# Kernel optimization log

Measured on AMD Instinct MI355X. Metric: run time of the kernel, lower is better.

## Reference

```python
import jax, jax.numpy as jnp
import numpy as np

HEATMAP_SIZE = 64

def _gauss5():
    n = np.array([[1, 4, 7, 4, 1],
                  [4, 16, 26, 16, 4],
                  [7, 26, 41, 26, 7],
                  [4, 16, 26, 16, 4],
                  [1, 4, 7, 4, 1]], dtype=np.float32) / 41.0
    return n

def setup_inputs() -> dict:
    key = jax.random.key(0)
    k1, k2, k3 = jax.random.split(key, 3)
    B, K = 1024, 24
    # coords in [-1.2, 1.2] so a few land out of the heatmap and exercise the masking path
    x = jax.random.uniform(k1, (B, K, 2), jnp.float32, -1.2, 1.2)
    # every (out,in) filter slice is the same 5x5 binomial gaussian (as in weights_init)
    weight = jnp.asarray(np.broadcast_to(_gauss5(), (K, K, 5, 5)).copy())
    vis_batch = jax.random.randint(k2, (256,), 0, B, jnp.int32)
    vis_kps = jax.random.randint(k3, (256,), 0, K, jnp.int32)
    return {"x": x, "weight": weight, "vis_batch": vis_batch, "vis_kps": vis_kps}

def _forward(x, weight, vis_batch, vis_kps):
    B, K, _ = x.shape
    H = HEATMAP_SIZE
    # j2d_resized = round((j2d + 1) / 2 * (H - 1)).long()
    coords = jnp.round((x + 1.0) * 0.5 * (H - 1)).astype(jnp.int32)  # [B,K,2] = (x,y)
    # rows with any out-of-range coord get both coords set to 0
    invalid = jnp.any((coords >= H) | (coords < 0), axis=-1)  # [B,K]
    coords = jnp.where(invalid[..., None], 0, coords)
    # torch quirk: only places a 1 where the x-coordinate is nonzero
    place = (coords[..., 0] != 0).astype(weight.dtype)  # [B,K]
    ohx = jax.nn.one_hot(coords[..., 0], H, dtype=weight.dtype)  # [B,K,H]
    ohy = jax.nn.one_hot(coords[..., 1], H, dtype=weight.dtype)  # [B,K,H]
    # sparse heatmap: 1 at (y, x)
    heat = place[..., None, None] * ohy[..., :, None] * ohx[..., None, :]  # [B,K,H,H]
    # heatmap[vis_batch, vis_kps, :, :] = 0
    kill = jnp.zeros((B, K), weight.dtype).at[vis_batch, vis_kps].set(1.0)
    heat = heat * (1.0 - kill)[..., None, None]
    # full 24->24 channel-mixing 5x5 conv, padding=2, no bias
    out = jax.lax.conv_general_dilated(
        heat, weight, window_strides=(1, 1), padding=((2, 2), (2, 2)),
        dimension_numbers=("NCHW", "OIHW", "NCHW"))
    return out

def reference(x, weight, vis_batch, vis_kps):
    return _forward(x, weight, vis_batch, vis_kps)
```

## Files before the change

### kernel.cpp

```cpp
#include <hip/hip_runtime.h>
#include <math.h>

#define B_SZ 1024
#define K_SZ 24
#define H_SZ 64
#define NVIS 256


__global__ __launch_bounds__(256) void gs_prep(
    const float2* __restrict__ x,
    const int*    __restrict__ vis_b,
    const int*    __restrict__ vis_k,
    int*          __restrict__ spike_tab)
{
    const int bk = blockIdx.x * 256 + threadIdx.x;
    const int b  = bk / K_SZ;
    const int k  = bk - b * K_SZ;
    const float2 c = x[bk];
    const int cx = (int)rintf((c.x + 1.0f) * 0.5f * 63.0f);
    const int cy = (int)rintf((c.y + 1.0f) * 0.5f * 63.0f);
    const bool ok = (cx >= 1) & (cx < H_SZ) & (cy >= 0) & (cy < H_SZ);
    int s = ok ? (cy * H_SZ + cx) : -1;
    for (int i = 0; i < NVIS; ++i) {
        if ((vis_b[i] == b) & (vis_k[i] == k)) s = -1;
    }
    spike_tab[bk] = s;
}

__global__ __launch_bounds__(256) void gs_main(
    const int*   __restrict__ spike_tab,
    const float* __restrict__ w,
    float*       __restrict__ out)
{
    __shared__ float tile[H_SZ * H_SZ];
    const int bid = blockIdx.x;
    const int b   = bid / K_SZ;
    const int o   = bid - b * K_SZ;
    const int tid = threadIdx.x;

    const int*   sp = spike_tab + b * K_SZ;
    const float* wo = w + o * (K_SZ * 25);
    int   sv[3]; float wv[3]; int pp[3];
    #pragma unroll
    for (int it = 0; it < 3; ++it) {
        const int t = tid + it * 256;
        if (t < K_SZ * 25) {
            const int c = t / 25;
            pp[it] = t - c * 25;
            sv[it] = sp[c];
            wv[it] = wo[t];
        } else {
            sv[it] = -1;
        }
    }

    float4* t4 = (float4*)tile;
    const float4 z = make_float4(0.f, 0.f, 0.f, 0.f);
    #pragma unroll
    for (int r = 0; r < 4; ++r) t4[r * 256 + tid] = z;
    __syncthreads();

    #pragma unroll
    for (int it = 0; it < 3; ++it) {
        const int s = sv[it];
        if (s >= 0) {
            const int y  = s >> 6;
            const int xx = s & 63;
            const int di = pp[it] / 5;
            const int dj = pp[it] - di * 5;
            const int i  = y + 2 - di;
            const int j  = xx + 2 - dj;
            if (((unsigned)i < H_SZ) & ((unsigned)j < H_SZ))
                atomicAdd(&tile[i * H_SZ + j], wv[it]);
        }
    }
    __syncthreads();

    float4* o4 = (float4*)(out + (size_t)bid * (H_SZ * H_SZ));
    #pragma unroll
    for (int r = 0; r < 4; ++r) o4[r * 256 + tid] = t4[r * 256 + tid];
}

extern "C" void kernel_launch(void* const* d_in, const int* in_sizes, int n_in,
                              void* d_out, int out_size, void* d_ws, size_t ws_size,
                              hipStream_t stream) {
    const float2* x     = (const float2*)d_in[0];
    const float*  w     = (const float*)d_in[1];
    const int*    vis_b = (const int*)d_in[2];
    const int*    vis_k = (const int*)d_in[3];
    float*        out   = (float*)d_out;
    int*          spike_tab = (int*)d_ws;

    gs_prep<<<(B_SZ * K_SZ) / 256, 256, 0, stream>>>(x, vis_b, vis_k, spike_tab);
    gs_main<<<B_SZ * K_SZ, 256, 0, stream>>>(spike_tab, w, out);
}
```

Measured before the change: 401.4 us.

## Process four output planes per block and stage kill list in shared memory

The main kernel now handles four output channels per block. It computes the spike scatter addresses once and reuses them across planes, zeroing and re-accumulating the shared tile for each plane. This cuts the block count by four and amortizes the address computation, but it adds extra barriers between planes. The prep kernel loads the kill list into shared memory as combined b*K+k indices, so each thread does one compare per entry instead of two global reads.

```diff
diff --git a/kernel.cpp b/kernel.cpp
--- a/kernel.cpp
+++ b/kernel.cpp
@@ -5,6 +5,7 @@
 #define K_SZ 24
 #define H_SZ 64
 #define NVIS 256
+#define PLANES 4
 
 
 __global__ __launch_bounds__(256) void gs_prep(
@@ -13,17 +14,19 @@
     const int*    __restrict__ vis_k,
     int*          __restrict__ spike_tab)
 {
-    const int bk = blockIdx.x * 256 + threadIdx.x;
-    const int b  = bk / K_SZ;
-    const int k  = bk - b * K_SZ;
+    __shared__ int kill[NVIS];
+    const int tid = threadIdx.x;
+    const int bk  = blockIdx.x * 256 + tid;
+    kill[tid] = vis_b[tid] * K_SZ + vis_k[tid];
     const float2 c = x[bk];
     const int cx = (int)rintf((c.x + 1.0f) * 0.5f * 63.0f);
     const int cy = (int)rintf((c.y + 1.0f) * 0.5f * 63.0f);
     const bool ok = (cx >= 1) & (cx < H_SZ) & (cy >= 0) & (cy < H_SZ);
     int s = ok ? (cy * H_SZ + cx) : -1;
-    for (int i = 0; i < NVIS; ++i) {
-        if ((vis_b[i] == b) & (vis_k[i] == k)) s = -1;
-    }
+    __syncthreads();
+#pragma unroll 16
+    for (int i = 0; i < NVIS; ++i)
+        if (kill[i] == bk) s = -1;
     spike_tab[bk] = s;
 }
 
@@ -34,51 +37,67 @@
 {
     __shared__ float tile[H_SZ * H_SZ];
     const int bid = blockIdx.x;
-    const int b   = bid / K_SZ;
-    const int o   = bid - b * K_SZ;
+    const int b   = bid / (K_SZ / PLANES);
+    const int o0  = (bid - b * (K_SZ / PLANES)) * PLANES;
     const int tid = threadIdx.x;
 
-    const int*   sp = spike_tab + b * K_SZ;
-    const float* wo = w + o * (K_SZ * 25);
-    int   sv[3]; float wv[3]; int pp[3];
-    #pragma unroll
+    const int* sp = spike_tab + b * K_SZ;
+    int addr[3];
+    int tt[3];
+#pragma unroll
     for (int it = 0; it < 3; ++it) {
         const int t = tid + it * 256;
+        addr[it] = -1;
+        tt[it]   = 0;
         if (t < K_SZ * 25) {
-            const int c = t / 25;
-            pp[it] = t - c * 25;
-            sv[it] = sp[c];
-            wv[it] = wo[t];
-        } else {
-            sv[it] = -1;
+            tt[it] = t;
+            const int c  = t / 25;
+            const int p  = t - c * 25;
+            const int s  = sp[c];
+            if (s >= 0) {
+                const int y  = s >> 6;
+                const int xx = s & 63;
+                const int di = p / 5;
+                const int dj = p - di * 5;
+                const int i  = y + 2 - di;
+                const int j  = xx + 2 - dj;
+                if (((unsigned)i < H_SZ) & ((unsigned)j < H_SZ))
+                    addr[it] = i * H_SZ + j;
+            }
         }
+    }
+
+    float wv[PLANES][3];
+#pragma unroll
+    for (int p = 0; p < PLANES; ++p) {
+        const float* wo = w + (o0 + p) * (K_SZ * 25);
+#pragma unroll
+        for (int it = 0; it < 3; ++it) wv[p][it] = wo[tt[it]];
     }
 
     float4* t4 = (float4*)tile;
     const float4 z = make_float4(0.f, 0.f, 0.f, 0.f);
-    #pragma unroll
+#pragma unroll
     for (int r = 0; r < 4; ++r) t4[r * 256 + tid] = z;
     __syncthreads();
 
-    #pragma unroll
-    for (int it = 0; it < 3; ++it) {
-        const int s = sv[it];
-        if (s >= 0) {
-            const int y  = s >> 6;
-            const int xx = s & 63;
-            const int di = pp[it] / 5;
-            const int dj = pp[it] - di * 5;
-            const int i  = y + 2 - di;
-            const int j  = xx + 2 - dj;
-            if (((unsigned)i < H_SZ) & ((unsigned)j < H_SZ))
-                atomicAdd(&tile[i * H_SZ + j], wv[it]);
+#pragma unroll
+    for (int p = 0; p < PLANES; ++p) {
+#pragma unroll
+        for (int it = 0; it < 3; ++it)
+            if (addr[it] >= 0) atomicAdd(&tile[addr[it]], wv[p][it]);
+        __syncthreads();
+
+        float4* o4 = (float4*)(out + ((size_t)(b * K_SZ + o0 + p) << 12));
+#pragma unroll
+        for (int r = 0; r < 4; ++r) {
+            const int idx = r * 256 + tid;
+            const float4 v = t4[idx];
+            o4[idx] = v;
+            if (p < PLANES - 1) t4[idx] = z;
         }
+        if (p < PLANES - 1) __syncthreads();
     }
-    __syncthreads();
-
-    float4* o4 = (float4*)(out + (size_t)bid * (H_SZ * H_SZ));
-    #pragma unroll
-    for (int r = 0; r < 4; ++r) o4[r * 256 + tid] = t4[r * 256 + tid];
 }
 
 extern "C" void kernel_launch(void* const* d_in, const int* in_sizes, int n_in,
@@ -92,5 +111,5 @@
     int*          spike_tab = (int*)d_ws;
 
     gs_prep<<<(B_SZ * K_SZ) / 256, 256, 0, stream>>>(x, vis_b, vis_k, spike_tab);
-    gs_main<<<B_SZ * K_SZ, 256, 0, stream>>>(spike_tab, w, out);
+    gs_main<<<B_SZ * (K_SZ / PLANES), 256, 0, stream>>>(spike_tab, w, out);
 }
```

New measurement: 408.1 us. About the same (+1.7%).
